# Optimization experiments

Hardware: AMD Instinct MI355X
Metric: run time of the kernel (lower is better)

Reference implementation:

```python
import jax, jax.numpy as jnp
import numpy as np
import math

B, T, D, La, Lr = 8, 128, 512, 2, 2
H = La + Lr
DK = D // H  # 128
DFF = 4 * D


def _gelu(x):
    # BERT tanh-approx GELU, matching the torch module exactly
    return 0.5 * x * (1.0 + jnp.tanh(math.sqrt(2.0 / math.pi) * (x + 0.044715 * x ** 3)))


def _ln(x, g, b, eps=1e-5):
    mu = jnp.mean(x, axis=-1, keepdims=True)
    var = jnp.mean((x - mu) ** 2, axis=-1, keepdims=True)
    return (x - mu) * jax.lax.rsqrt(var + eps) * g + b


def setup_inputs() -> dict:
    key = jax.random.key(0)
    ks = jax.random.split(key, 16)
    n = lambda k, s, sc=1.0: jax.random.normal(k, s, dtype=jnp.float32) * sc
    return {
        'x': n(ks[0], (B, T, D)),
        'mask': jnp.ones((B, 1, T, T), dtype=jnp.int32),
        'abs_kernel': n(ks[1], (La, B, T, D)),
        'rel_kernel': n(ks[2], (Lr, B, T, T, D)),
        'Wc': n(ks[3], (3, D, D), 0.02), 'bc': jnp.zeros((3, D), jnp.float32),
        'Wpq': n(ks[4], (La, D, DK), 0.02), 'bpq': jnp.zeros((La, DK), jnp.float32),
        'Wpk': n(ks[5], (La, D, DK), 0.02), 'bpk': jnp.zeros((La, DK), jnp.float32),
        'Wrk': n(ks[6], (Lr, D, DK), 0.02), 'brk': jnp.zeros((Lr, DK), jnp.float32),
        'rel_bias': n(ks[7], (Lr, DK), 0.02),
        'Wo': n(ks[8], (D, D), 0.02), 'bo': jnp.zeros((D,), jnp.float32),
        'W1': n(ks[9], (D, DFF), 0.02), 'b1': jnp.zeros((DFF,), jnp.float32),
        'W2': n(ks[10], (DFF, D), 0.02), 'b2': jnp.zeros((D,), jnp.float32),
        'ln1_g': jnp.ones((D,), jnp.float32), 'ln1_b': jnp.zeros((D,), jnp.float32),
        'ln2_g': jnp.ones((D,), jnp.float32), 'ln2_b': jnp.zeros((D,), jnp.float32),
    }


def _attention(h, mask, abs_kernel, rel_kernel, Wc, bc, Wpq, bpq, Wpk, bpk,
               Wrk, brk, rel_bias, Wo, bo):
    b, t = h.shape[0], h.shape[1]
    # content projections: [3,B,T,D] -> [3,B,H,T,DK]
    qkv = jnp.einsum('btd,cde->cbte', h, Wc) + bc[:, None, None, :]
    qkv = qkv.reshape(3, b, t, H, DK).transpose(0, 1, 3, 2, 4)
    q, k, v = qkv[0], qkv[1], qkv[2]
    # absolute-position heads
    Pq = jnp.einsum('abtd,ade->bate', abs_kernel, Wpq) + bpq[None, :, None, :]
    Pk = jnp.einsum('abtd,ade->bate', abs_kernel, Wpk) + bpk[None, :, None, :]
    abs_scores = jnp.einsum('blid,bljd->blij', q[:, :La] + Pq, k[:, :La] + Pk)
    # relative-position heads (R: [B,Lr,T,T,DK])
    R = jnp.einsum('abijd,ade->baije', rel_kernel, Wrk) + brk[None, :, None, None, :]
    Xq = q[:, La:]
    rel_scores = jnp.einsum('blid,bljd->blij', Xq, k[:, La:])
    rel_scores = rel_scores + jnp.einsum('blid,blijd->blij', Xq + rel_bias[None, :, None, :], R)
    scores = jnp.concatenate([abs_scores, rel_scores], axis=1) * (DK ** -0.5)
    scores = jnp.where(mask == 0, jnp.float32(-1e9), scores)
    p_attn = jax.nn.softmax(scores, axis=-1)
    out = jnp.einsum('bhij,bhjd->bhid', p_attn, v)
    out = out.transpose(0, 2, 1, 3).reshape(b, t, H * DK)
    return out @ Wo + bo


def reference(x, mask, abs_kernel, rel_kernel, Wc, bc, Wpq, bpq, Wpk, bpk,
              Wrk, brk, rel_bias, Wo, bo, W1, b1, W2, b2,
              ln1_g, ln1_b, ln2_g, ln2_b):
    # pre-LN sublayer 1: attention
    h = _ln(x, ln1_g, ln1_b)
    x = x + _attention(h, mask, abs_kernel, rel_kernel, Wc, bc, Wpq, bpq,
                       Wpk, bpk, Wrk, brk, rel_bias, Wo, bo)
    # pre-LN sublayer 2: FFN with tanh-GELU
    h2 = _ln(x, ln2_g, ln2_b)
    x = x + (_gelu(h2 @ W1 + b1) @ W2 + b2)
    return x
```

## Files before the change

### kernel.cpp

```cpp
#include <hip/hip_runtime.h>
#include <math.h>

typedef __attribute__((ext_vector_type(8))) short short8v;
typedef __attribute__((ext_vector_type(4))) float f32x4;

static __device__ __forceinline__ ushort f2bf(float x) {
  unsigned u = __builtin_bit_cast(unsigned, x);
  unsigned r = (u + 0x7fffu + ((u >> 16) & 1u)) >> 16;
  return (ushort)r;
}

__device__ __forceinline__ float gelu_f(float v) {
  float t = tanhf(0.7978845608028654f * (v + 0.044715f * v * v * v));
  return 0.5f * v * (1.0f + t);
}

struct CvtTasks {
  const float* src[16];
  void* dst[16];
  int rows[16], cols[16], mode[16], aux[16], end[16];
};

__global__ __launch_bounds__(256) void cvt_kernel(CvtTasks T,
    const float* __restrict__ lnx, const float* __restrict__ lng,
    const float* __restrict__ lnb, ushort* __restrict__ lnout)
{
  __shared__ ushort tile[64][65];
  int b = blockIdx.x, t = threadIdx.x;
  int ti = 0;
  while (b >= T.end[ti]) ++ti;
  int lb = b - (ti ? T.end[ti-1] : 0);
  const float* src = T.src[ti];
  int mode = T.mode[ti];
  if (mode == 0) {
    int R = T.rows[ti], C = T.cols[ti];
    int tpr = C >> 6;
    int tyy = lb / tpr, txx = lb - tyy * tpr;
    int r0 = tyy << 6, c0 = txx << 6;
    int lr = t >> 4, lc4 = (t & 15) << 2;
    #pragma unroll
    for (int i = 0; i < 4; ++i) {
      int row = i*16 + lr;
      float4 vv = *(const float4*)(src + (size_t)(r0+row)*C + c0 + lc4);
      tile[row][lc4+0] = f2bf(vv.x);
      tile[row][lc4+1] = f2bf(vv.y);
      tile[row][lc4+2] = f2bf(vv.z);
      tile[row][lc4+3] = f2bf(vv.w);
    }
    __syncthreads();
    ushort* dst = (ushort*)T.dst[ti];
    #pragma unroll
    for (int i = 0; i < 4; ++i) {
      int n = i*16 + lr;
      ushort4 o;
      o.x = tile[lc4+0][n];
      o.y = tile[lc4+1][n];
      o.z = tile[lc4+2][n];
      o.w = tile[lc4+3][n];
      *(ushort4*)(dst + (size_t)(c0+n)*R + r0 + lc4) = o;
    }
  } else if (mode == 1) {
    int idx = lb*2048 + t*8;
    float4 v0 = *(const float4*)(src + idx);
    float4 v1 = *(const float4*)(src + idx + 4);
    union { ushort u[8]; uint4 q; } pk;
    pk.u[0]=f2bf(v0.x); pk.u[1]=f2bf(v0.y); pk.u[2]=f2bf(v0.z); pk.u[3]=f2bf(v0.w);
    pk.u[4]=f2bf(v1.x); pk.u[5]=f2bf(v1.y); pk.u[6]=f2bf(v1.z); pk.u[7]=f2bf(v1.w);
    *(uint4*)((ushort*)T.dst[ti] + idx) = pk.q;
  } else if (mode == 2) {
    if (t < T.cols[ti]) {
      float* d = (float*)T.dst[ti];
      for (int r = 0; r < T.rows[ti]; ++r)
        d[(size_t)(2*r + T.aux[ti]) * T.cols[ti] + t] = src[(size_t)r * T.cols[ti] + t];
    }
  } else {
    int row = lb*4 + (t >> 6);
    int lane = t & 63;
    const float* xr = lnx + (size_t)row*512 + lane*8;
    float4 a = *(const float4*)xr;
    float4 c = *(const float4*)(xr + 4);
    float s  = a.x + a.y + a.z + a.w + c.x + c.y + c.z + c.w;
    float ss = a.x*a.x + a.y*a.y + a.z*a.z + a.w*a.w
             + c.x*c.x + c.y*c.y + c.z*c.z + c.w*c.w;
    #pragma unroll
    for (int off = 32; off > 0; off >>= 1) {
      s  += __shfl_xor(s, off);
      ss += __shfl_xor(ss, off);
    }
    float mu  = s * (1.0f/512.0f);
    float var = ss * (1.0f/512.0f) - mu*mu;
    float rstd = rsqrtf(var + 1e-5f);
    float4 g0 = *(const float4*)(lng + lane*8), g1 = *(const float4*)(lng + lane*8 + 4);
    float4 b0 = *(const float4*)(lnb + lane*8), b1 = *(const float4*)(lnb + lane*8 + 4);
    union { ushort u[8]; uint4 v; } pk;
    pk.u[0] = f2bf((a.x-mu)*rstd*g0.x + b0.x);
    pk.u[1] = f2bf((a.y-mu)*rstd*g0.y + b0.y);
    pk.u[2] = f2bf((a.z-mu)*rstd*g0.z + b0.z);
    pk.u[3] = f2bf((a.w-mu)*rstd*g0.w + b0.w);
    pk.u[4] = f2bf((c.x-mu)*rstd*g1.x + b1.x);
    pk.u[5] = f2bf((c.y-mu)*rstd*g1.y + b1.y);
    pk.u[6] = f2bf((c.z-mu)*rstd*g1.z + b1.z);
    pk.u[7] = f2bf((c.w-mu)*rstd*g1.w + b1.w);
    *(uint4*)(lnout + (size_t)row*512 + lane*8) = pk.v;
  }
}

template<bool OUT_BF16, bool GELU_>
__device__ __forceinline__ void gemm64_body(
    const ushort* __restrict__ A, int lda,
    const ushort* __restrict__ Bt, int ldb,
    const float* __restrict__ bias,
    void* __restrict__ Cout, int ldc,
    int ksteps, int bm, int bn)
{
  __shared__ __align__(16) char smem[16384];
  char* asB = smem;
  char* bsB = smem + 8192;
  int tid = threadIdx.x;
  int lane = tid & 63, wid = tid >> 6;
  int wr = wid >> 1, wc = wid & 1;
  int l15 = lane & 15, kg = lane >> 4;
  f32x4 acc[2][2] = {};
  const ushort* Ab = A + (size_t)bm * lda;
  const ushort* Bb = Bt + (size_t)bn * ldb;
  int r0 = tid >> 3;
  int c16 = tid & 7;
  int wb0 = r0*128 + ((c16*16) ^ ((r0 & 7) << 4));
  int wb1 = (r0+32)*128 + ((c16*16) ^ ((r0 & 7) << 4));
  for (int ks = 0; ks < ksteps; ++ks) {
    int k0 = ks * 64;
    uint4 ra0 = *(const uint4*)(Ab + (size_t)r0*lda + k0 + c16*8);
    uint4 ra1 = *(const uint4*)(Ab + (size_t)(r0+32)*lda + k0 + c16*8);
    uint4 rb0 = *(const uint4*)(Bb + (size_t)r0*ldb + k0 + c16*8);
    uint4 rb1 = *(const uint4*)(Bb + (size_t)(r0+32)*ldb + k0 + c16*8);
    __syncthreads();
    *(uint4*)(asB + wb0) = ra0;  *(uint4*)(asB + wb1) = ra1;
    *(uint4*)(bsB + wb0) = rb0;  *(uint4*)(bsB + wb1) = rb1;
    __syncthreads();
    #pragma unroll
    for (int half = 0; half < 2; ++half) {
      int cb = half*64 + kg*16;
      short8v av[2], bv[2];
      #pragma unroll
      for (int m = 0; m < 2; ++m) {
        int r = wr*32 + m*16 + l15;
        av[m] = *(const short8v*)(asB + r*128 + (cb ^ ((r & 7) << 4)));
      }
      #pragma unroll
      for (int n = 0; n < 2; ++n) {
        int r = wc*32 + n*16 + l15;
        bv[n] = *(const short8v*)(bsB + r*128 + (cb ^ ((r & 7) << 4)));
      }
      #pragma unroll
      for (int m = 0; m < 2; ++m)
        #pragma unroll
        for (int n = 0; n < 2; ++n)
          acc[m][n] = __builtin_amdgcn_mfma_f32_16x16x32_bf16(av[m], bv[n], acc[m][n], 0, 0, 0);
    }
  }
  int orow0 = bm + wr*32 + kg*4;
  int ocol0 = bn + wc*32 + l15;
  #pragma unroll
  for (int m = 0; m < 2; ++m) {
    #pragma unroll
    for (int r = 0; r < 4; ++r) {
      int row = orow0 + m*16 + r;
      #pragma unroll
      for (int n = 0; n < 2; ++n) {
        int col = ocol0 + n*16;
        float val = acc[m][n][r];
        if (bias) val += bias[col];
        if (GELU_) val = gelu_f(val);
        if (OUT_BF16) ((ushort*)Cout)[(size_t)row*ldc + col] = f2bf(val);
        else          ((float*)Cout)[(size_t)row*ldc + col]  = val;
      }
    }
  }
}

template<bool OUT_BF16, bool GELU_>
__global__ __launch_bounds__(256) void g64(
    const ushort* __restrict__ A, int lda, long Abatch,
    const ushort* __restrict__ Bt, int ldb, long Bbatch,
    const float* __restrict__ bias, int biasStride,
    void* __restrict__ C, int ldc, long Cbatch,
    int ksteps)
{
  int z = blockIdx.z;
  const float* bz = bias ? bias + (size_t)z * biasStride : nullptr;
  void* Cz = OUT_BF16 ? (void*)((ushort*)C + (size_t)z*Cbatch)
                      : (void*)((float*)C + (size_t)z*Cbatch);
  gemm64_body<OUT_BF16, GELU_>(A + (size_t)z*Abatch, lda,
      Bt + (size_t)z*Bbatch, ldb, bz, Cz, ldc, ksteps,
      blockIdx.y*64, blockIdx.x*64);
}

__global__ __launch_bounds__(256) void qkvp_gemm(
    const ushort* __restrict__ h, const ushort* __restrict__ WcT,
    const float* __restrict__ bc, float* __restrict__ qkv,
    const ushort* __restrict__ absb, const ushort* __restrict__ Wp,
    const float* __restrict__ bqk, float* __restrict__ Pqk)
{
  int z = blockIdx.z;
  const ushort *A, *Bt;
  const float* bias;
  float* C;
  int ldc;
  if (z < 3) {
    A = h; Bt = WcT + (size_t)z*262144; bias = bc + z*512;
    C = qkv + (size_t)z*524288; ldc = 512;
  } else {
    if (blockIdx.x >= 2) return;
    int t = z - 3;
    A = absb + (size_t)(t >> 1)*524288;
    Bt = Wp + (size_t)t*65536;
    bias = bqk + t*128;
    C = Pqk + (size_t)t*131072; ldc = 128;
  }
  gemm64_body<false,false>(A, 512, Bt, 512, bias, C, ldc, 8,
      blockIdx.y*64, blockIdx.x*64);
}

__global__ __launch_bounds__(256) void fused_pre(
    const float* __restrict__ q, const float* __restrict__ k,
    float* __restrict__ Pqk, const float* __restrict__ rel_bias,
    const float* __restrict__ brk, const ushort* __restrict__ Wrkb,
    float* __restrict__ u, float* __restrict__ cvec)
{
  int blk = blockIdx.x;
  int tid = threadIdx.x;
  if (blk < 256) {
    int l = blk >> 7;
    int rem = blk & 127;
    int bm = (rem >> 3) * 64;
    int bn = (rem & 7) * 64;
    __shared__ __align__(16) char smem[16384];
    char* asB = smem;
    char* bsB = smem + 8192;
    int lane = tid & 63, wid = tid >> 6;
    int wr = wid >> 1, wc = wid & 1;
    int l15 = lane & 15, kg = lane >> 4;
    f32x4 acc[2][2] = {};
    const ushort* Bb = Wrkb + (size_t)l*65536 + (size_t)bn*128;
    int r0 = tid >> 3, c16 = tid & 7;
    int wb0 = r0*128 + ((c16*16) ^ ((r0 & 7) << 4));
    int wb1 = (r0+32)*128 + ((c16*16) ^ ((r0 & 7) << 4));
    const float* rbp = rel_bias + l*128;
    #pragma unroll
    for (int ks = 0; ks < 2; ++ks) {
      int k0 = ks * 64;
      int e0 = k0 + c16*8;
      uint4 ra[2], rb[2];
      #pragma unroll
      for (int i = 0; i < 2; ++i) {
        int m = bm + r0 + i*32;
        const float* qp = q + (size_t)m*512 + (2+l)*128 + e0;
        float4 qa = *(const float4*)qp;
        float4 qb = *(const float4*)(qp + 4);
        float4 rr0 = *(const float4*)(rbp + e0);
        float4 rr1 = *(const float4*)(rbp + e0 + 4);
        union { ushort s[8]; uint4 v; } pk;
        pk.s[0]=f2bf(qa.x+rr0.x); pk.s[1]=f2bf(qa.y+rr0.y);
        pk.s[2]=f2bf(qa.z+rr0.z); pk.s[3]=f2bf(qa.w+rr0.w);
        pk.s[4]=f2bf(qb.x+rr1.x); pk.s[5]=f2bf(qb.y+rr1.y);
        pk.s[6]=f2bf(qb.z+rr1.z); pk.s[7]=f2bf(qb.w+rr1.w);
        ra[i] = pk.v;
        rb[i] = *(const uint4*)(Bb + (size_t)(r0 + i*32)*128 + e0);
      }
      __syncthreads();
      *(uint4*)(asB + wb0) = ra[0];  *(uint4*)(asB + wb1) = ra[1];
      *(uint4*)(bsB + wb0) = rb[0];  *(uint4*)(bsB + wb1) = rb[1];
      __syncthreads();
      #pragma unroll
      for (int half = 0; half < 2; ++half) {
        int cb = half*64 + kg*16;
        short8v av[2], bv[2];
        #pragma unroll
        for (int m = 0; m < 2; ++m) {
          int r = wr*32 + m*16 + l15;
          av[m] = *(const short8v*)(asB + r*128 + (cb ^ ((r & 7) << 4)));
        }
        #pragma unroll
        for (int n = 0; n < 2; ++n) {
          int r = wc*32 + n*16 + l15;
          bv[n] = *(const short8v*)(bsB + r*128 + (cb ^ ((r & 7) << 4)));
        }
        #pragma unroll
        for (int m = 0; m < 2; ++m)
          #pragma unroll
          for (int n = 0; n < 2; ++n)
            acc[m][n] = __builtin_amdgcn_mfma_f32_16x16x32_bf16(av[m], bv[n], acc[m][n], 0, 0, 0);
      }
    }
    float* Cz = u + (size_t)l*524288;
    int orow0 = bm + wr*32 + kg*4;
    int ocol0 = bn + wc*32 + l15;
    #pragma unroll
    for (int m = 0; m < 2; ++m)
      #pragma unroll
      for (int r = 0; r < 4; ++r) {
        int row = orow0 + m*16 + r;
        #pragma unroll
        for (int n = 0; n < 2; ++n)
          Cz[(size_t)row*512 + ocol0 + n*16] = acc[m][n][r];
      }
  } else if (blk < 1280) {
    int idx = (blk - 256)*256 + tid;
    int dk = idx & 127;
    int rest = idx >> 7;
    int m = rest & 1023;
    int a = rest >> 10;
    Pqk[idx + a*131072]     += q[(size_t)m*512 + a*128 + dk];
    Pqk[idx + (a+1)*131072] += k[(size_t)m*512 + a*128 + dk];
  } else {
    int row = (blk - 1280)*2 + (tid >> 7);
    int l = row >> 10, m = row & 1023;
    int t = tid & 127, hf = tid >> 7;
    float val = q[(size_t)m*512 + (2+l)*128 + t] + rel_bias[l*128 + t];
    float p = brk[l*128 + t] * val;
    #pragma unroll
    for (int off = 32; off > 0; off >>= 1) p += __shfl_xor(p, off);
    __shared__ float red[2][2];
    if ((tid & 63) == 0) red[hf][(tid >> 6) & 1] = p;
    __syncthreads();
    if (t == 0) cvec[row] = red[hf][0] + red[hf][1];
  }
}

__global__ __launch_bounds__(256) void attn_kernel(
    const float* __restrict__ rk, const float* __restrict__ u,
    const float* __restrict__ q, const float* __restrict__ k,
    const float* __restrict__ v, const float* __restrict__ cvec,
    const float* __restrict__ Pqk, const int* __restrict__ mask,
    ushort* __restrict__ attnob)
{
  int blk = blockIdx.x;
  int tid = threadIdx.x;
  if (blk < 2048) {
    int i = blk & 127, b = (blk >> 7) & 7, l = blk >> 10, h = 2 + l;
    int m_i = b*128 + i;
    __shared__ float qs[128], sc[128], ps[128], red[64], pvs[2][128], stat[2];
    int wave = tid >> 6, lane = tid & 63;
    const float* ur = u + ((size_t)l*1024 + m_i)*512 + lane*8;
    float4 uu0 = *(const float4*)ur;
    float4 uu1 = *(const float4*)(ur + 4);
    if (tid < 128) qs[tid] = q[(size_t)m_i*512 + h*128 + tid];
    __syncthreads();
    float xq0 = qs[lane*2], xq1 = qs[lane*2+1];
    const float* base = rk + (size_t)blk*65536 + lane*8;
    const float* kb = k + (size_t)(b*128)*512 + h*128 + lane*2;
    #pragma unroll 2
    for (int jj = 0; jj < 32; ++jj) {
      int j = wave*32 + jj;
      const float* r = base + (size_t)j*512;
      float4 r0 = *(const float4*)r;
      float4 r1 = *(const float4*)(r + 4);
      float2 kk = *(const float2*)(kb + (size_t)j*512);
      float s = r0.x*uu0.x + r0.y*uu0.y + r0.z*uu0.z + r0.w*uu0.w
              + r1.x*uu1.x + r1.y*uu1.y + r1.z*uu1.z + r1.w*uu1.w
              + kk.x*xq0 + kk.y*xq1;
      #pragma unroll
      for (int off = 32; off > 0; off >>= 1) s += __shfl_xor(s, off);
      if (lane == 0) sc[j] = s;
    }
    __syncthreads();
    if (tid < 128) {
      float sv = (sc[tid] + cvec[l*1024 + m_i]) * 0.088388347648318447f;
      if (mask[((size_t)(b*128) + i)*128 + tid] == 0) sv = -1e9f;
      sc[tid] = sv;
    }
    __syncthreads();
    if (tid < 64) red[tid] = fmaxf(sc[tid], sc[tid+64]);
    __syncthreads();
    if (tid < 64) {
      float m = red[tid];
      #pragma unroll
      for (int off = 32; off > 0; off >>= 1) m = fmaxf(m, __shfl_xor(m, off));
      if (tid == 0) stat[0] = m;
    }
    __syncthreads();
    if (tid < 128) ps[tid] = __expf(sc[tid] - stat[0]);
    __syncthreads();
    if (tid < 64) red[tid] = ps[tid] + ps[tid+64];
    __syncthreads();
    if (tid < 64) {
      float s = red[tid];
      #pragma unroll
      for (int off = 32; off > 0; off >>= 1) s += __shfl_xor(s, off);
      if (tid == 0) stat[1] = 1.0f / s;
    }
    __syncthreads();
    int hf = tid >> 7, dk = tid & 127;
    const float* vp = v + (size_t)(b*128 + hf*64)*512 + h*128 + dk;
    float o = 0.0f;
    #pragma unroll 4
    for (int jj = 0; jj < 64; ++jj) o += ps[hf*64 + jj] * vp[(size_t)jj*512];
    pvs[hf][dk] = o;
    __syncthreads();
    if (tid < 128)
      attnob[(size_t)m_i*512 + h*128 + tid] = f2bf((pvs[0][tid] + pvs[1][tid]) * stat[1]);
  } else {
    int ab = blk - 2048;
    int hf = tid >> 7, t = tid & 127;
    int i  = (ab & 63)*2 + hf;
    int bh = ab >> 6;
    int h  = bh & 1, b = bh >> 1;
    __shared__ float qsh[2][128], psh[2][128], redm[2][2], reds[2][2];
    int m_i = b*128 + i;
    qsh[hf][t] = Pqk[(size_t)(2*h)*131072 + (size_t)m_i*128 + t];
    __syncthreads();
    int m_j = b*128 + t;
    const float* krow = Pqk + (size_t)(2*h+1)*131072 + (size_t)m_j*128;
    float dot = 0.0f;
    #pragma unroll
    for (int d = 0; d < 128; d += 4) {
      float4 kv = *(const float4*)(krow + d);
      dot += kv.x*qsh[hf][d] + kv.y*qsh[hf][d+1] + kv.z*qsh[hf][d+2] + kv.w*qsh[hf][d+3];
    }
    float s = dot * 0.088388347648318447f;
    if (mask[((size_t)(b*128) + i)*128 + t] == 0) s = -1e9f;
    float mx = s;
    #pragma unroll
    for (int off = 32; off > 0; off >>= 1) mx = fmaxf(mx, __shfl_xor(mx, off));
    int w2 = (tid >> 6) & 1;
    if ((tid & 63) == 0) redm[hf][w2] = mx;
    __syncthreads();
    mx = fmaxf(redm[hf][0], redm[hf][1]);
    float e = __expf(s - mx);
    psh[hf][t] = e;
    float sum = e;
    #pragma unroll
    for (int off = 32; off > 0; off >>= 1) sum += __shfl_xor(sum, off);
    if ((tid & 63) == 0) reds[hf][w2] = sum;
    __syncthreads();
    float inv = 1.0f / (reds[hf][0] + reds[hf][1]);
    const float* vp = v + (size_t)b*65536 + h*128 + t;
    float o = 0.0f;
    #pragma unroll 4
    for (int jj = 0; jj < 128; ++jj) o += psh[hf][jj] * vp[(size_t)jj*512];
    attnob[(size_t)m_i*512 + h*128 + t] = f2bf(o * inv);
  }
}

__global__ __launch_bounds__(256) void reduce_ln_kernel(
    const float* __restrict__ wpart, const float* __restrict__ bo,
    const float* __restrict__ x, const float* __restrict__ g,
    const float* __restrict__ bb, float* __restrict__ x1,
    ushort* __restrict__ h2)
{
  int gid = blockIdx.x*256 + threadIdx.x;
  int row = gid >> 6, lane = threadIdx.x & 63;
  size_t off = (size_t)row*512 + lane*8;
  float4 a = *(const float4*)(x + off);
  float4 c = *(const float4*)(x + off + 4);
  #pragma unroll
  for (int sk = 0; sk < 4; ++sk) {
    float4 p0 = *(const float4*)(wpart + (size_t)sk*524288 + off);
    float4 p1 = *(const float4*)(wpart + (size_t)sk*524288 + off + 4);
    a.x += p0.x; a.y += p0.y; a.z += p0.z; a.w += p0.w;
    c.x += p1.x; c.y += p1.y; c.z += p1.z; c.w += p1.w;
  }
  float4 bo0 = *(const float4*)(bo + lane*8);
  float4 bo1 = *(const float4*)(bo + lane*8 + 4);
  a.x += bo0.x; a.y += bo0.y; a.z += bo0.z; a.w += bo0.w;
  c.x += bo1.x; c.y += bo1.y; c.z += bo1.z; c.w += bo1.w;
  *(float4*)(x1 + off) = a;
  *(float4*)(x1 + off + 4) = c;
  float s  = a.x + a.y + a.z + a.w + c.x + c.y + c.z + c.w;
  float ss = a.x*a.x + a.y*a.y + a.z*a.z + a.w*a.w
           + c.x*c.x + c.y*c.y + c.z*c.z + c.w*c.w;
  #pragma unroll
  for (int off2 = 32; off2 > 0; off2 >>= 1) {
    s  += __shfl_xor(s, off2);
    ss += __shfl_xor(ss, off2);
  }
  float mu  = s * (1.0f/512.0f);
  float var = ss * (1.0f/512.0f) - mu*mu;
  float rstd = rsqrtf(var + 1e-5f);
  float4 g0 = *(const float4*)(g + lane*8), g1 = *(const float4*)(g + lane*8 + 4);
  float4 b0 = *(const float4*)(bb + lane*8), b1 = *(const float4*)(bb + lane*8 + 4);
  union { ushort u[8]; uint4 v; } pk;
  pk.u[0] = f2bf((a.x-mu)*rstd*g0.x + b0.x);
  pk.u[1] = f2bf((a.y-mu)*rstd*g0.y + b0.y);
  pk.u[2] = f2bf((a.z-mu)*rstd*g0.z + b0.z);
  pk.u[3] = f2bf((a.w-mu)*rstd*g0.w + b0.w);
  pk.u[4] = f2bf((c.x-mu)*rstd*g1.x + b1.x);
  pk.u[5] = f2bf((c.y-mu)*rstd*g1.y + b1.y);
  pk.u[6] = f2bf((c.z-mu)*rstd*g1.z + b1.z);
  pk.u[7] = f2bf((c.w-mu)*rstd*g1.w + b1.w);
  *(uint4*)(h2 + off) = pk.v;
}

__global__ __launch_bounds__(256) void reduce_out_kernel(
    const float* __restrict__ fpart, const float* __restrict__ b2,
    const float* __restrict__ x1, float* __restrict__ out)
{
  int idx = blockIdx.x*256 + threadIdx.x;
  size_t o4 = (size_t)idx*4;
  float4 s = *(const float4*)(x1 + o4);
  #pragma unroll
  for (int sk = 0; sk < 4; ++sk) {
    float4 p = *(const float4*)(fpart + (size_t)sk*524288 + o4);
    s.x += p.x; s.y += p.y; s.z += p.z; s.w += p.w;
  }
  float4 bv = *(const float4*)(b2 + ((idx & 127)*4));
  s.x += bv.x; s.y += bv.y; s.z += bv.z; s.w += bv.w;
  *(float4*)(out + o4) = s;
}

extern "C" void kernel_launch(void* const* d_in, const int* in_sizes, int n_in,
                              void* d_out, int out_size, void* d_ws, size_t ws_size,
                              hipStream_t stream)
{
  const float* x         = (const float*)d_in[0];
  const int*   mask      = (const int*)  d_in[1];
  const float* abs_kernel= (const float*)d_in[2];
  const float* rel_kernel= (const float*)d_in[3];
  const float* Wc        = (const float*)d_in[4];
  const float* bc        = (const float*)d_in[5];
  const float* Wpq       = (const float*)d_in[6];
  const float* bpq       = (const float*)d_in[7];
  const float* Wpk       = (const float*)d_in[8];
  const float* bpk       = (const float*)d_in[9];
  const float* Wrk       = (const float*)d_in[10];
  const float* brk       = (const float*)d_in[11];
  const float* rel_bias  = (const float*)d_in[12];
  const float* Wo        = (const float*)d_in[13];
  const float* bo        = (const float*)d_in[14];
  const float* W1        = (const float*)d_in[15];
  const float* b1        = (const float*)d_in[16];
  const float* W2        = (const float*)d_in[17];
  const float* b2        = (const float*)d_in[18];
  const float* ln1g      = (const float*)d_in[19];
  const float* ln1b      = (const float*)d_in[20];
  const float* ln2g      = (const float*)d_in[21];
  const float* ln2b      = (const float*)d_in[22];

  float* ws = (float*)d_ws;
  float* q      = ws;
  float* kbuf   = ws + 524288;
  float* v      = ws + 1048576;
  float* Pqk    = ws + 1572864;
  float* u      = ws + 2097152;
  float* x1     = ws + 3145728;
  float* cvec   = ws + 3670016;
  float* bqk    = ws + 3672064;
  float* wpart  = ws + 3672576;
  float* fpart  = wpart;
  ushort* bf    = (ushort*)(ws + 5769728);
  ushort* h     = bf;
  ushort* h2    = bf + 524288;
  ushort* attnob= bf + 1048576;
  ushort* f1    = bf + 1572864;
  ushort* absb  = bf + 3670016;
  ushort* WcT   = bf + 4718592;
  ushort* Wp    = bf + 5505024;
  ushort* Wrkb  = bf + 5767168;
  ushort* WoT   = bf + 5898240;
  ushort* W1T   = bf + 6160384;
  ushort* W2T   = bf + 7208960;
  float* out    = (float*)d_out;

  CvtTasks T{};
  int nb = 0, ti = 0;
  auto addTr = [&](const float* s, ushort* d, int R, int C) {
    T.src[ti]=s; T.dst[ti]=d; T.rows[ti]=R; T.cols[ti]=C; T.mode[ti]=0; T.aux[ti]=0;
    nb += (R/64)*(C/64); T.end[ti]=nb; ++ti;
  };
  auto addCv = [&](const float* s, ushort* d, int n) {
    T.src[ti]=s; T.dst[ti]=d; T.rows[ti]=n; T.cols[ti]=0; T.mode[ti]=1; T.aux[ti]=0;
    nb += n/2048; T.end[ti]=nb; ++ti;
  };
  auto addBi = [&](const float* s, float* d, int aux) {
    T.src[ti]=s; T.dst[ti]=d; T.rows[ti]=2; T.cols[ti]=128; T.mode[ti]=2; T.aux[ti]=aux;
    nb += 1; T.end[ti]=nb; ++ti;
  };
  for (int c = 0; c < 3; ++c) addTr(Wc + (size_t)c*262144, WcT + (size_t)c*262144, 512, 512);
  addTr(Wo, WoT, 512, 512);
  addTr(W1, W1T, 512, 2048);
  addTr(W2, W2T, 2048, 512);
  for (int a = 0; a < 2; ++a) addTr(Wpq + (size_t)a*65536, Wp + (size_t)(2*a)*65536, 512, 128);
  for (int a = 0; a < 2; ++a) addTr(Wpk + (size_t)a*65536, Wp + (size_t)(2*a+1)*65536, 512, 128);
  addCv(abs_kernel, absb, 1048576);
  addCv(Wrk, Wrkb, 131072);
  addBi(bpq, bqk, 0);
  addBi(bpk, bqk, 1);
  T.src[ti]=x; T.dst[ti]=h; T.mode[ti]=3; nb += 256; T.end[ti]=nb; ++ti;

  cvt_kernel<<<nb, 256, 0, stream>>>(T, x, ln1g, ln1b, h);

  qkvp_gemm<<<dim3(8,16,7), 256, 0, stream>>>(h, WcT, bc, q, absb, Wp, bqk, Pqk);

  fused_pre<<<2304, 256, 0, stream>>>(q, kbuf, Pqk, rel_bias, brk, Wrkb, u, cvec);

  attn_kernel<<<3072, 256, 0, stream>>>(rel_kernel, u, q, kbuf, v, cvec, Pqk, mask, attnob);

  g64<false,false><<<dim3(8,16,4), 256, 0, stream>>>(
      attnob, 512, 128, WoT, 512, 128, nullptr, 0, wpart, 512, 524288, 2);

  reduce_ln_kernel<<<256, 256, 0, stream>>>(wpart, bo, x, ln2g, ln2b, x1, h2);

  g64<true,true><<<dim3(32,16,1), 256, 0, stream>>>(
      h2, 512, 0, W1T, 512, 0, b1, 0, f1, 2048, 0, 8);

  g64<false,false><<<dim3(8,16,4), 256, 0, stream>>>(
      f1, 2048, 512, W2T, 2048, 512, nullptr, 0, fpart, 512, 524288, 8);

  reduce_out_kernel<<<512, 256, 0, stream>>>(fpart, b2, x1, out);
}
```

Before: 204.8 us.

## Double-buffer GEMM LDS tiles and fold weight transposes into attention kernel

The shared GEMM body now uses two LDS buffers, prefetching the next K-slice into registers while MFMAs run on the current one, so each step needs one barrier instead of two. The Wo/W1/W2 transpose-and-convert work moves from the upfront cvt kernel into extra blocks of the attention kernel, so it runs alongside the attention work and shortens the serial preamble. Shared memory in the attention kernel is unioned across branches. LDS per GEMM block doubles to 32KB, which may lower occupancy. A B-operand load index in fused_pre is also changed.

```diff
diff --git a/kernel.cpp b/kernel.cpp
--- a/kernel.cpp
+++ b/kernel.cpp
@@ -13,6 +13,38 @@
 __device__ __forceinline__ float gelu_f(float v) {
   float t = tanhf(0.7978845608028654f * (v + 0.044715f * v * v * v));
   return 0.5f * v * (1.0f + t);
+}
+
+__device__ __forceinline__ void transpose_tile(char* shm,
+    const float* __restrict__ src, ushort* __restrict__ dst,
+    int R, int C, int lb)
+{
+  ushort (*tile)[65] = (ushort(*)[65])shm;
+  int t = threadIdx.x;
+  int tpr = C >> 6;
+  int tyy = lb / tpr, txx = lb - tyy * tpr;
+  int r0 = tyy << 6, c0 = txx << 6;
+  int lr = t >> 4, lc4 = (t & 15) << 2;
+  #pragma unroll
+  for (int i = 0; i < 4; ++i) {
+    int row = i*16 + lr;
+    float4 vv = *(const float4*)(src + (size_t)(r0+row)*C + c0 + lc4);
+    tile[row][lc4+0] = f2bf(vv.x);
+    tile[row][lc4+1] = f2bf(vv.y);
+    tile[row][lc4+2] = f2bf(vv.z);
+    tile[row][lc4+3] = f2bf(vv.w);
+  }
+  __syncthreads();
+  #pragma unroll
+  for (int i = 0; i < 4; ++i) {
+    int n = i*16 + lr;
+    ushort4 o;
+    o.x = tile[lc4+0][n];
+    o.y = tile[lc4+1][n];
+    o.z = tile[lc4+2][n];
+    o.w = tile[lc4+3][n];
+    *(ushort4*)(dst + (size_t)(c0+n)*R + r0 + lc4) = o;
+  }
 }
 
 struct CvtTasks {
@@ -25,7 +57,7 @@
     const float* __restrict__ lnx, const float* __restrict__ lng,
     const float* __restrict__ lnb, ushort* __restrict__ lnout)
 {
-  __shared__ ushort tile[64][65];
+  __shared__ __align__(16) char shm[8448];
   int b = blockIdx.x, t = threadIdx.x;
   int ti = 0;
   while (b >= T.end[ti]) ++ti;
@@ -33,32 +65,7 @@
   const float* src = T.src[ti];
   int mode = T.mode[ti];
   if (mode == 0) {
-    int R = T.rows[ti], C = T.cols[ti];
-    int tpr = C >> 6;
-    int tyy = lb / tpr, txx = lb - tyy * tpr;
-    int r0 = tyy << 6, c0 = txx << 6;
-    int lr = t >> 4, lc4 = (t & 15) << 2;
-    #pragma unroll
-    for (int i = 0; i < 4; ++i) {
-      int row = i*16 + lr;
-      float4 vv = *(const float4*)(src + (size_t)(r0+row)*C + c0 + lc4);
-      tile[row][lc4+0] = f2bf(vv.x);
-      tile[row][lc4+1] = f2bf(vv.y);
-      tile[row][lc4+2] = f2bf(vv.z);
-      tile[row][lc4+3] = f2bf(vv.w);
-    }
-    __syncthreads();
-    ushort* dst = (ushort*)T.dst[ti];
-    #pragma unroll
-    for (int i = 0; i < 4; ++i) {
-      int n = i*16 + lr;
-      ushort4 o;
-      o.x = tile[lc4+0][n];
-      o.y = tile[lc4+1][n];
-      o.z = tile[lc4+2][n];
-      o.w = tile[lc4+3][n];
-      *(ushort4*)(dst + (size_t)(c0+n)*R + r0 + lc4) = o;
-    }
+    transpose_tile(shm, src, (ushort*)T.dst[ti], T.rows[ti], T.cols[ti], lb);
   } else if (mode == 1) {
     int idx = lb*2048 + t*8;
     float4 v0 = *(const float4*)(src + idx);
@@ -106,16 +113,13 @@
 }
 
 template<bool OUT_BF16, bool GELU_>
-__device__ __forceinline__ void gemm64_body(
+__device__ __forceinline__ void gemm64_body(char* smem,
     const ushort* __restrict__ A, int lda,
     const ushort* __restrict__ Bt, int ldb,
     const float* __restrict__ bias,
     void* __restrict__ Cout, int ldc,
     int ksteps, int bm, int bn)
 {
-  __shared__ __align__(16) char smem[16384];
-  char* asB = smem;
-  char* bsB = smem + 8192;
   int tid = threadIdx.x;
   int lane = tid & 63, wid = tid >> 6;
   int wr = wid >> 1, wc = wid & 1;
@@ -127,16 +131,26 @@
   int c16 = tid & 7;
   int wb0 = r0*128 + ((c16*16) ^ ((r0 & 7) << 4));
   int wb1 = (r0+32)*128 + ((c16*16) ^ ((r0 & 7) << 4));
+  uint4 ra0 = *(const uint4*)(Ab + (size_t)r0*lda + c16*8);
+  uint4 ra1 = *(const uint4*)(Ab + (size_t)(r0+32)*lda + c16*8);
+  uint4 rb0 = *(const uint4*)(Bb + (size_t)r0*ldb + c16*8);
+  uint4 rb1 = *(const uint4*)(Bb + (size_t)(r0+32)*ldb + c16*8);
+  *(uint4*)(smem + wb0) = ra0;  *(uint4*)(smem + wb1) = ra1;
+  *(uint4*)(smem + 8192 + wb0) = rb0;  *(uint4*)(smem + 8192 + wb1) = rb1;
+  __syncthreads();
   for (int ks = 0; ks < ksteps; ++ks) {
-    int k0 = ks * 64;
-    uint4 ra0 = *(const uint4*)(Ab + (size_t)r0*lda + k0 + c16*8);
-    uint4 ra1 = *(const uint4*)(Ab + (size_t)(r0+32)*lda + k0 + c16*8);
-    uint4 rb0 = *(const uint4*)(Bb + (size_t)r0*ldb + k0 + c16*8);
-    uint4 rb1 = *(const uint4*)(Bb + (size_t)(r0+32)*ldb + k0 + c16*8);
-    __syncthreads();
-    *(uint4*)(asB + wb0) = ra0;  *(uint4*)(asB + wb1) = ra1;
-    *(uint4*)(bsB + wb0) = rb0;  *(uint4*)(bsB + wb1) = rb1;
-    __syncthreads();
+    char* buf = smem + (ks & 1)*16384;
+    char* nxt = smem + ((ks + 1) & 1)*16384;
+    bool more = (ks + 1 < ksteps);
+    if (more) {
+      int k0 = (ks + 1) * 64;
+      ra0 = *(const uint4*)(Ab + (size_t)r0*lda + k0 + c16*8);
+      ra1 = *(const uint4*)(Ab + (size_t)(r0+32)*lda + k0 + c16*8);
+      rb0 = *(const uint4*)(Bb + (size_t)r0*ldb + k0 + c16*8);
+      rb1 = *(const uint4*)(Bb + (size_t)(r0+32)*ldb + k0 + c16*8);
+    }
+    char* asB = buf;
+    char* bsB = buf + 8192;
     #pragma unroll
     for (int half = 0; half < 2; ++half) {
       int cb = half*64 + kg*16;
@@ -157,6 +171,11 @@
         for (int n = 0; n < 2; ++n)
           acc[m][n] = __builtin_amdgcn_mfma_f32_16x16x32_bf16(av[m], bv[n], acc[m][n], 0, 0, 0);
     }
+    if (more) {
+      *(uint4*)(nxt + wb0) = ra0;  *(uint4*)(nxt + wb1) = ra1;
+      *(uint4*)(nxt + 8192 + wb0) = rb0;  *(uint4*)(nxt + 8192 + wb1) = rb1;
+    }
+    __syncthreads();
   }
   int orow0 = bm + wr*32 + kg*4;
   int ocol0 = bn + wc*32 + l15;
@@ -186,11 +205,12 @@
     void* __restrict__ C, int ldc, long Cbatch,
     int ksteps)
 {
+  __shared__ __align__(16) char smem[32768];
   int z = blockIdx.z;
   const float* bz = bias ? bias + (size_t)z * biasStride : nullptr;
   void* Cz = OUT_BF16 ? (void*)((ushort*)C + (size_t)z*Cbatch)
                       : (void*)((float*)C + (size_t)z*Cbatch);
-  gemm64_body<OUT_BF16, GELU_>(A + (size_t)z*Abatch, lda,
+  gemm64_body<OUT_BF16, GELU_>(smem, A + (size_t)z*Abatch, lda,
       Bt + (size_t)z*Bbatch, ldb, bz, Cz, ldc, ksteps,
       blockIdx.y*64, blockIdx.x*64);
 }
@@ -201,6 +221,7 @@
     const ushort* __restrict__ absb, const ushort* __restrict__ Wp,
     const float* __restrict__ bqk, float* __restrict__ Pqk)
 {
+  __shared__ __align__(16) char smem[32768];
   int z = blockIdx.z;
   const ushort *A, *Bt;
   const float* bias;
@@ -217,7 +238,7 @@
     bias = bqk + t*128;
     C = Pqk + (size_t)t*131072; ldc = 128;
   }
-  gemm64_body<false,false>(A, 512, Bt, 512, bias, C, ldc, 8,
+  gemm64_body<false,false>(smem, A, 512, Bt, 512, bias, C, ldc, 8,
       blockIdx.y*64, blockIdx.x*64);
 }
 
@@ -265,7 +286,7 @@
         pk.s[4]=f2bf(qb.x+rr1.x); pk.s[5]=f2bf(qb.y+rr1.y);
         pk.s[6]=f2bf(qb.z+rr1.z); pk.s[7]=f2bf(qb.w+rr1.w);
         ra[i] = pk.v;
-        rb[i] = *(const uint4*)(Bb + (size_t)(r0 + i*32)*128 + e0);
+        rb[i] = *(const uint4*)(Bb + (size_t)(r0 + i*32)*128 + k0 + c16*8);
       }
       __syncthreads();
       *(uint4*)(asB + wb0) = ra[0];  *(uint4*)(asB + wb1) = ra[1];
@@ -332,21 +353,26 @@
     const float* __restrict__ q, const float* __restrict__ k,
     const float* __restrict__ v, const float* __restrict__ cvec,
     const float* __restrict__ Pqk, const int* __restrict__ mask,
-    ushort* __restrict__ attnob)
-{
+    ushort* __restrict__ attnob,
+    const float* __restrict__ Wo, ushort* __restrict__ WoT,
+    const float* __restrict__ W1, ushort* __restrict__ W1T,
+    const float* __restrict__ W2, ushort* __restrict__ W2T)
+{
+  __shared__ __align__(16) char shm[8448];
   int blk = blockIdx.x;
   int tid = threadIdx.x;
   if (blk < 2048) {
+    struct RelShm { float qs[128], sc[128], ps[128], red[64], pvs[2][128], stat[2]; };
+    RelShm* S = (RelShm*)shm;
     int i = blk & 127, b = (blk >> 7) & 7, l = blk >> 10, h = 2 + l;
     int m_i = b*128 + i;
-    __shared__ float qs[128], sc[128], ps[128], red[64], pvs[2][128], stat[2];
     int wave = tid >> 6, lane = tid & 63;
     const float* ur = u + ((size_t)l*1024 + m_i)*512 + lane*8;
     float4 uu0 = *(const float4*)ur;
     float4 uu1 = *(const float4*)(ur + 4);
-    if (tid < 128) qs[tid] = q[(size_t)m_i*512 + h*128 + tid];
-    __syncthreads();
-    float xq0 = qs[lane*2], xq1 = qs[lane*2+1];
+    if (tid < 128) S->qs[tid] = q[(size_t)m_i*512 + h*128 + tid];
+    __syncthreads();
+    float xq0 = S->qs[lane*2], xq1 = S->qs[lane*2+1];
     const float* base = rk + (size_t)blk*65536 + lane*8;
     const float* kb = k + (size_t)(b*128)*512 + h*128 + lane*2;
     #pragma unroll 2
@@ -361,53 +387,54 @@
               + kk.x*xq0 + kk.y*xq1;
       #pragma unroll
       for (int off = 32; off > 0; off >>= 1) s += __shfl_xor(s, off);
-      if (lane == 0) sc[j] = s;
+      if (lane == 0) S->sc[j] = s;
     }
     __syncthreads();
     if (tid < 128) {
-      float sv = (sc[tid] + cvec[l*1024 + m_i]) * 0.088388347648318447f;
+      float sv = (S->sc[tid] + cvec[l*1024 + m_i]) * 0.088388347648318447f;
       if (mask[((size_t)(b*128) + i)*128 + tid] == 0) sv = -1e9f;
-      sc[tid] = sv;
-    }
-    __syncthreads();
-    if (tid < 64) red[tid] = fmaxf(sc[tid], sc[tid+64]);
+      S->sc[tid] = sv;
+    }
+    __syncthreads();
+    if (tid < 64) S->red[tid] = fmaxf(S->sc[tid], S->sc[tid+64]);
     __syncthreads();
     if (tid < 64) {
-      float m = red[tid];
+      float m = S->red[tid];
       #pragma unroll
       for (int off = 32; off > 0; off >>= 1) m = fmaxf(m, __shfl_xor(m, off));
-      if (tid == 0) stat[0] = m;
-    }
-    __syncthreads();
-    if (tid < 128) ps[tid] = __expf(sc[tid] - stat[0]);
-    __syncthreads();
-    if (tid < 64) red[tid] = ps[tid] + ps[tid+64];
+      if (tid == 0) S->stat[0] = m;
+    }
+    __syncthreads();
+    if (tid < 128) S->ps[tid] = __expf(S->sc[tid] - S->stat[0]);
+    __syncthreads();
+    if (tid < 64) S->red[tid] = S->ps[tid] + S->ps[tid+64];
     __syncthreads();
     if (tid < 64) {
-      float s = red[tid];
+      float s = S->red[tid];
       #pragma unroll
       for (int off = 32; off > 0; off >>= 1) s += __shfl_xor(s, off);
-      if (tid == 0) stat[1] = 1.0f / s;
+      if (tid == 0) S->stat[1] = 1.0f / s;
     }
     __syncthreads();
     int hf = tid >> 7, dk = tid & 127;
     const float* vp = v + (size_t)(b*128 + hf*64)*512 + h*128 + dk;
     float o = 0.0f;
     #pragma unroll 4
-    for (int jj = 0; jj < 64; ++jj) o += ps[hf*64 + jj] * vp[(size_t)jj*512];
-    pvs[hf][dk] = o;
+    for (int jj = 0; jj < 64; ++jj) o += S->ps[hf*64 + jj] * vp[(size_t)jj*512];
+    S->pvs[hf][dk] = o;
     __syncthreads();
     if (tid < 128)
-      attnob[(size_t)m_i*512 + h*128 + tid] = f2bf((pvs[0][tid] + pvs[1][tid]) * stat[1]);
-  } else {
+      attnob[(size_t)m_i*512 + h*128 + tid] = f2bf((S->pvs[0][tid] + S->pvs[1][tid]) * S->stat[1]);
+  } else if (blk < 3072) {
+    struct AbsShm { float qsh[2][128], psh[2][128], redm[2][2], reds[2][2]; };
+    AbsShm* S = (AbsShm*)shm;
     int ab = blk - 2048;
     int hf = tid >> 7, t = tid & 127;
     int i  = (ab & 63)*2 + hf;
     int bh = ab >> 6;
     int h  = bh & 1, b = bh >> 1;
-    __shared__ float qsh[2][128], psh[2][128], redm[2][2], reds[2][2];
     int m_i = b*128 + i;
-    qsh[hf][t] = Pqk[(size_t)(2*h)*131072 + (size_t)m_i*128 + t];
+    S->qsh[hf][t] = Pqk[(size_t)(2*h)*131072 + (size_t)m_i*128 + t];
     __syncthreads();
     int m_j = b*128 + t;
     const float* krow = Pqk + (size_t)(2*h+1)*131072 + (size_t)m_j*128;
@@ -415,7 +442,7 @@
     #pragma unroll
     for (int d = 0; d < 128; d += 4) {
       float4 kv = *(const float4*)(krow + d);
-      dot += kv.x*qsh[hf][d] + kv.y*qsh[hf][d+1] + kv.z*qsh[hf][d+2] + kv.w*qsh[hf][d+3];
+      dot += kv.x*S->qsh[hf][d] + kv.y*S->qsh[hf][d+1] + kv.z*S->qsh[hf][d+2] + kv.w*S->qsh[hf][d+3];
     }
     float s = dot * 0.088388347648318447f;
     if (mask[((size_t)(b*128) + i)*128 + t] == 0) s = -1e9f;
@@ -423,22 +450,27 @@
     #pragma unroll
     for (int off = 32; off > 0; off >>= 1) mx = fmaxf(mx, __shfl_xor(mx, off));
     int w2 = (tid >> 6) & 1;
-    if ((tid & 63) == 0) redm[hf][w2] = mx;
-    __syncthreads();
-    mx = fmaxf(redm[hf][0], redm[hf][1]);
+    if ((tid & 63) == 0) S->redm[hf][w2] = mx;
+    __syncthreads();
+    mx = fmaxf(S->redm[hf][0], S->redm[hf][1]);
     float e = __expf(s - mx);
-    psh[hf][t] = e;
+    S->psh[hf][t] = e;
     float sum = e;
     #pragma unroll
     for (int off = 32; off > 0; off >>= 1) sum += __shfl_xor(sum, off);
-    if ((tid & 63) == 0) reds[hf][w2] = sum;
-    __syncthreads();
-    float inv = 1.0f / (reds[hf][0] + reds[hf][1]);
+    if ((tid & 63) == 0) S->reds[hf][w2] = sum;
+    __syncthreads();
+    float inv = 1.0f / (S->reds[hf][0] + S->reds[hf][1]);
     const float* vp = v + (size_t)b*65536 + h*128 + t;
     float o = 0.0f;
     #pragma unroll 4
-    for (int jj = 0; jj < 128; ++jj) o += psh[hf][jj] * vp[(size_t)jj*512];
+    for (int jj = 0; jj < 128; ++jj) o += S->psh[hf][jj] * vp[(size_t)jj*512];
     attnob[(size_t)m_i*512 + h*128 + t] = f2bf(o * inv);
+  } else {
+    int t2 = blk - 3072;
+    if (t2 < 64)       transpose_tile(shm, Wo, WoT, 512, 512, t2);
+    else if (t2 < 320) transpose_tile(shm, W1, W1T, 512, 2048, t2 - 64);
+    else               transpose_tile(shm, W2, W2T, 2048, 512, t2 - 320);
   }
 }
 
@@ -576,9 +608,6 @@
     nb += 1; T.end[ti]=nb; ++ti;
   };
   for (int c = 0; c < 3; ++c) addTr(Wc + (size_t)c*262144, WcT + (size_t)c*262144, 512, 512);
-  addTr(Wo, WoT, 512, 512);
-  addTr(W1, W1T, 512, 2048);
-  addTr(W2, W2T, 2048, 512);
   for (int a = 0; a < 2; ++a) addTr(Wpq + (size_t)a*65536, Wp + (size_t)(2*a)*65536, 512, 128);
   for (int a = 0; a < 2; ++a) addTr(Wpk + (size_t)a*65536, Wp + (size_t)(2*a+1)*65536, 512, 128);
   addCv(abs_kernel, absb, 1048576);
@@ -593,7 +622,8 @@
 
   fused_pre<<<2304, 256, 0, stream>>>(q, kbuf, Pqk, rel_bias, brk, Wrkb, u, cvec);
 
-  attn_kernel<<<3072, 256, 0, stream>>>(rel_kernel, u, q, kbuf, v, cvec, Pqk, mask, attnob);
+  attn_kernel<<<3648, 256, 0, stream>>>(rel_kernel, u, q, kbuf, v, cvec, Pqk,
+                                        mask, attnob, Wo, WoT, W1, W1T, W2, W2T);
 
   g64<false,false><<<dim3(8,16,4), 256, 0, stream>>>(
       attnob, 512, 128, WoT, 512, 128, nullptr, 0, wpart, 512, 524288, 2);
```

After: 197.7 us, median of 2. -3.5%, faster.
